# Kernel optimization log

Measured on AMD Instinct MI355X. Metric: run time of the kernel, lower is better.

The kernel has to match this reference:

```python
import jax, jax.numpy as jnp
import numpy as np
from jax import lax

H = 16          # num heads
D_CONV = 4      # causal conv kernel width
NORMALIZER = 16.0
EPS = 1e-5


def _causal_conv_silu(x, w):
    # x: [B, L, D], w: [D, W] depthwise causal conv, then silu
    B, L, D = x.shape
    xp = jnp.pad(x, ((0, 0), (D_CONV - 1, 0), (0, 0)))
    y = sum(xp[:, k:k + L, :] * w[:, k] for k in range(D_CONV))
    return jax.nn.silu(y)


def _gla_scan(q, k, v, gk):
    # q,k,gk: [B,H,L,dk]; v: [B,H,L,dv]
    B, h, L, dk = q.shape
    dv = v.shape[-1]
    qT = jnp.moveaxis(q, 2, 0)
    kT = jnp.moveaxis(k, 2, 0)
    vT = jnp.moveaxis(v, 2, 0)
    gT = jnp.moveaxis(gk, 2, 0)

    def step(S, inp):
        qt, kt, vt, gt = inp  # [B,H,dk] / [B,H,dv]
        S = S * jnp.exp(gt)[..., None] + kt[..., None] * vt[..., None, :]
        ot = jnp.einsum('bhk,bhkv->bhv', qt, S)
        return S, ot

    S0 = jnp.zeros((B, h, dk, dv), q.dtype)
    S, o = lax.scan(step, S0, (qT, kT, vT, gT))
    return jnp.moveaxis(o, 0, 2), S  # [B,H,L,dv], final state


def setup_inputs() -> dict:
    key = jax.random.key(0)
    ks = jax.random.split(key, 9)
    L, B, D = 8192, 8, 1024
    s = lambda fan: 1.0 / np.sqrt(fan)
    return {
        'x': jax.random.normal(ks[0], (L, B, D), jnp.float32),
        'conv_w': jax.random.normal(ks[1], (D, D_CONV), jnp.float32) * s(D_CONV),
        'Wq': jax.random.normal(ks[2], (D, D // 2), jnp.float32) * s(D),
        'Wkg': jax.random.normal(ks[3], (D, D // 2), jnp.float32) * s(D),
        'Wv': jax.random.normal(ks[4], (D, D), jnp.float32) * s(D),
        'Wg': jax.random.normal(ks[5], (D, D), jnp.float32) * s(D),
        'bg': jax.random.normal(ks[6], (D,), jnp.float32) * 0.02,
        'Wout': jax.random.normal(ks[7], (D, D), jnp.float32) * s(D),
        'aug_balance': jnp.zeros((D // 2,), jnp.float32),
    }


def reference(x, conv_w, Wq, Wkg, Wv, Wg, bg, Wout, aug_balance):
    # x: [L, B, D] -> [B, L, D]
    xb = jnp.swapaxes(x, 0, 1)
    xb = _causal_conv_silu(xb, conv_w)

    q = xb @ Wq                      # [B,L,D/2]
    k_gate = xb @ Wkg                # [B,L,D/2]
    v = xb @ Wv                      # [B,L,D]
    g = xb @ Wg + bg                 # [B,L,D]

    gk = jax.nn.log_sigmoid(k_gate) / NORMALIZER
    k = 1.0 - jnp.exp(gk)

    B, L, _ = q.shape
    split = lambda t: t.reshape(B, L, H, -1).transpose(0, 2, 1, 3)  # b h l d
    qh, kh, gkh, vh = split(q), split(k), split(gk), split(v)
    dk = qh.shape[-1]

    # fused_chunk_gla default scale = dk ** -0.5 (applied to q internally)
    o, new_state = _gla_scan(qh * (dk ** -0.5), kh, vh, gkh)

    # meta self-augmentation (uses unscaled q)
    aug = aug_balance.reshape(H, dk)
    aug_w = jnp.einsum('bhlk,hk,bhlk->bhl', qh, aug, kh)
    o = o + jax.nn.sigmoid(aug_w[..., None] * vh)

    # group norm: LayerNorm over head_dim, no affine
    mu = o.mean(-1, keepdims=True)
    var = o.var(-1, keepdims=True)
    o = (o - mu) * lax.rsqrt(var + EPS)

    o = o.transpose(0, 2, 1, 3).reshape(B, L, -1)  # [B,L,D]
    out = (jax.nn.silu(g) * o) @ Wout
    return jnp.swapaxes(out, 0, 1), new_state  # [L,B,D], [B,H,dk,dv]
```

## Files before the change

### kernel.cpp

```cpp
#include <hip/hip_runtime.h>
#include <stdint.h>

typedef __attribute__((ext_vector_type(4))) float f32x4;
typedef _Float16 f16x8 __attribute__((ext_vector_type(8)));
typedef __attribute__((ext_vector_type(8))) unsigned short u16x8;
typedef __attribute__((ext_vector_type(2))) unsigned int u32x2;
typedef unsigned short u16;
typedef unsigned int u32;

#define LSEQ 8192
#define BB 8
#define DD 1024
#define MM 65536
#define NCH 128

__device__ __forceinline__ u16 f2h(float f) {
    _Float16 h = (_Float16)f;
    return *(u16*)&h;
}
__device__ __forceinline__ float h2f(u16 u) {
    _Float16 h = *(_Float16*)&u;
    return (float)h;
}

__device__ __forceinline__ void gload_lds16(const void* g, void* l) {
    __builtin_amdgcn_global_load_lds(
        (const __attribute__((address_space(1))) u32*)g,
        (__attribute__((address_space(3))) u32*)l, 16, 0, 0);
}

__global__ __launch_bounds__(256) void k_conv_silu(const float* __restrict__ x,
                                                   const float* __restrict__ w,
                                                   u16* __restrict__ xb) {
    int m = blockIdx.x;
    int b = m >> 13, l = m & 8191;
    int d0 = threadIdx.x * 4;
    f32x4 wv[4];
#pragma unroll
    for (int j = 0; j < 4; j++) wv[j] = *(const f32x4*)&w[(d0 + j) * 4];
    float acc[4] = {0.f, 0.f, 0.f, 0.f};
#pragma unroll
    for (int kk = 0; kk < 4; kk++) {
        int lp = l - 3 + kk;
        if (lp >= 0) {
            f32x4 xv = *(const f32x4*)&x[((size_t)(lp * BB + b)) * DD + d0];
#pragma unroll
            for (int j = 0; j < 4; j++) acc[j] += xv[j] * wv[j][kk];
        }
    }
    u16 o[4];
#pragma unroll
    for (int j = 0; j < 4; j++) {
        float a = acc[j];
        o[j] = f2h(a / (1.f + __expf(-a)));
    }
    u32x2 pk;
    pk.x = (u32)o[0] | ((u32)o[1] << 16);
    pk.y = (u32)o[2] | ((u32)o[3] << 16);
    *(u32x2*)&xb[(size_t)m * DD + d0] = pk;
}

__global__ __launch_bounds__(256) void k_packW(const float* __restrict__ Wq,
                                               const float* __restrict__ Wkg,
                                               const float* __restrict__ Wv,
                                               const float* __restrict__ Wg,
                                               const float* __restrict__ Wout,
                                               u16* __restrict__ Wcat,
                                               u16* __restrict__ WoutT) {
    int idx = blockIdx.x * 256 + threadIdx.x;
    const int T1 = 3072 * 1024;
    if (idx < T1) {
        int n = idx >> 10, kk = idx & 1023;
        float v;
        if (n < 512)        v = Wq [kk * 512 + n];
        else if (n < 1024)  v = Wkg[kk * 512 + (n - 512)];
        else if (n < 2048)  v = Wv [kk * 1024 + (n - 1024)];
        else                v = Wg [kk * 1024 + (n - 2048)];
        Wcat[idx] = f2h(v);
    } else {
        int j = idx - T1;
        if (j < 1024 * 1024) {
            int n = j >> 10, kk = j & 1023;
            WoutT[j] = f2h(Wout[kk * 1024 + n]);
        }
    }
}

template <int MODE>
__device__ __forceinline__ void epi_frag(f32x4 v, int grow0, int gcol,
                                         u16* __restrict__ qo, u16* __restrict__ gko,
                                         u16* __restrict__ ko, u16* __restrict__ vo,
                                         u16* __restrict__ sgo, const float* __restrict__ bg,
                                         float* __restrict__ out) {
#pragma unroll
    for (int rr = 0; rr < 4; rr++) {
        int grow = grow0 + rr;
        float val = v[rr];
        if (MODE == 1) {
            if (gcol < 512) {
                qo[(size_t)grow * 512 + gcol] = f2h(val);
            } else if (gcol < 1024) {
                float ls = fminf(val, 0.f) - log1pf(__expf(-fabsf(val)));
                float gkv = ls * 0.0625f;
                gko[(size_t)grow * 512 + (gcol - 512)] = f2h(gkv);
                ko [(size_t)grow * 512 + (gcol - 512)] = f2h(-expm1f(gkv));
            } else if (gcol < 2048) {
                vo[(size_t)grow * 1024 + (gcol - 1024)] = f2h(val);
            } else {
                float gg = val + bg[gcol - 2048];
                sgo[(size_t)grow * 1024 + (gcol - 2048)] = f2h(gg / (1.f + __expf(-gg)));
            }
        } else {
            int l = grow & 8191, b = grow >> 13;
            out[((size_t)(l * BB + b)) * DD + gcol] = val;
        }
    }
}

template <int MODE>
__global__ __launch_bounds__(256, 3) void k_gemm_bt(
    const u16* __restrict__ A, const u16* __restrict__ Bt, int nt_tiles,
    u16* __restrict__ qo, u16* __restrict__ gko, u16* __restrict__ ko,
    u16* __restrict__ vo, u16* __restrict__ sgo, const float* __restrict__ bg,
    float* __restrict__ out) {
    const int K = 1024;
    __shared__ __align__(16) u16 Sm[20480];
    int tid = threadIdx.x;
    int w = tid >> 6, lane = tid & 63;
    int wm = w >> 1, wn = w & 1;
    int lr = lane & 15, lk = lane >> 4;

    int xcd = blockIdx.x & 7;
    int cidx = blockIdx.x >> 3;
    int grpsz = nt_tiles * 4;
    int grp = cidx / grpsz;
    int r = cidx - grp * grpsz;
    int ntile = r >> 2;
    int mts_per_chunk = (gridDim.x >> 3) / nt_tiles;
    int mtile = xcd * mts_per_chunk + grp * 4 + (r & 3);
    int m0 = mtile << 8, n0 = ntile << 6;

#define DECL_ACC(MT) f32x4 a##MT##_0 = {0.f,0.f,0.f,0.f}, a##MT##_1 = {0.f,0.f,0.f,0.f};
    DECL_ACC(0) DECL_ACC(1) DECL_ACC(2) DECL_ACC(3)
    DECL_ACC(4) DECL_ACC(5) DECL_ACC(6) DECL_ACC(7)
#undef DECL_ACC

    int row = tid >> 2;
    int sslot = (tid & 3) ^ ((tid >> 3) & 3);
    const u16* gA = A + (size_t)(m0 + row) * K + sslot * 8;
    const u16* gB = Bt + (size_t)(n0 + row) * K + sslot * 8;
    char* lA = (char*)Sm + w * 1024;
    char* lB = (char*)Sm + 16384 + w * 1024;

#define STAGE(TT, OB) { \
    int k1 = (TT) << 5; \
    gload_lds16(gA + k1, lA + (OB)); \
    gload_lds16(gA + (size_t)64 * K + k1, lA + (OB) + 4096); \
    gload_lds16(gA + (size_t)128 * K + k1, lA + (OB) + 8192); \
    gload_lds16(gA + (size_t)192 * K + k1, lA + (OB) + 12288); \
    gload_lds16(gB + k1, lB + (OB)); }

#define MFMA_ROW(MT) { \
    f16x8 av = *(const f16x8*)&As[(wm * 128 + MT * 16 + lr) * 32 + acsl]; \
    a##MT##_0 = __builtin_amdgcn_mfma_f32_16x16x32_f16(av, b0, a##MT##_0, 0, 0, 0); \
    a##MT##_1 = __builtin_amdgcn_mfma_f32_16x16x32_f16(av, b1, a##MT##_1, 0, 0, 0); }

#define COMPUTE() { \
    int acsl = (lk ^ ((lr >> 1) & 3)) * 8; \
    f16x8 b0 = *(const f16x8*)&Bs[(wn * 32 +  0 + lr) * 32 + acsl]; \
    f16x8 b1 = *(const f16x8*)&Bs[(wn * 32 + 16 + lr) * 32 + acsl]; \
    __builtin_amdgcn_s_setprio(1); \
    MFMA_ROW(0) MFMA_ROW(1) MFMA_ROW(2) MFMA_ROW(3) \
    MFMA_ROW(4) MFMA_ROW(5) MFMA_ROW(6) MFMA_ROW(7) \
    __builtin_amdgcn_s_setprio(0); }

    STAGE(0, 0)
    STAGE(1, 20480)

    for (int t = 0; t < 31; ++t) {
        asm volatile("s_waitcnt vmcnt(5)" ::: "memory");
        __builtin_amdgcn_sched_barrier(0);
        __builtin_amdgcn_s_barrier();
        {
            const u16* As = Sm + (t & 1) * 10240;
            const u16* Bs = As + 8192;
            COMPUTE()
        }
        __builtin_amdgcn_s_barrier();
        __builtin_amdgcn_sched_barrier(0);
        if (t < 30) {
            STAGE(t + 2, (t & 1) * 20480)
        }
    }
    asm volatile("s_waitcnt vmcnt(0)" ::: "memory");
    __builtin_amdgcn_sched_barrier(0);
    __builtin_amdgcn_s_barrier();
    {
        const u16* As = Sm + 10240;
        const u16* Bs = As + 8192;
        COMPUTE()
    }
#undef COMPUTE
#undef MFMA_ROW
#undef STAGE

#define EPI_ROW(MT) { \
    int gr0 = m0 + wm * 128 + MT * 16 + lk * 4; \
    epi_frag<MODE>(a##MT##_0, gr0, n0 + wn * 32 +  0 + lr, qo, gko, ko, vo, sgo, bg, out); \
    epi_frag<MODE>(a##MT##_1, gr0, n0 + wn * 32 + 16 + lr, qo, gko, ko, vo, sgo, bg, out); }
    EPI_ROW(0) EPI_ROW(1) EPI_ROW(2) EPI_ROW(3)
    EPI_ROW(4) EPI_ROW(5) EPI_ROW(6) EPI_ROW(7)
#undef EPI_ROW
}

__global__ __launch_bounds__(64) void k_pass1(const u16* __restrict__ gkb,
                                              const u16* __restrict__ kb,
                                              const u16* __restrict__ vb,
                                              float* __restrict__ Mo,
                                              float* __restrict__ eGC) {
    __shared__ __align__(16) float kkT[64 * 32];
    int bhc = blockIdx.x;
    int c = bhc & 127, bh = bhc >> 7;
    int h = bh & 15, b = bh >> 4;
    int m0 = b * LSEQ + c * 64;
    int lane = threadIdx.x;
    if (lane < 32) {
        int i = lane;
        size_t base = (size_t)m0 * 512 + h * 32 + i;
        float G = 0.f;
        for (int t = 0; t < 64; t++) {
            G += h2f(gkb[base + (size_t)t * 512]);
            G = fmaxf(G, -60.f);
            kkT[t * 32 + i] = h2f(kb[base + (size_t)t * 512]) * __expf(-G);
        }
        eGC[bhc * 32 + i] = __expf(G);
    }
    __syncthreads();
    float Ma[32];
#pragma unroll
    for (int i = 0; i < 32; i++) Ma[i] = 0.f;
    size_t vbase = (size_t)m0 * 1024 + h * 64 + lane;
    for (int t = 0; t < 64; t++) {
        float vj = h2f(vb[vbase + (size_t)t * 1024]);
#pragma unroll
        for (int i4 = 0; i4 < 32; i4 += 4) {
            f32x4 kk4 = *(const f32x4*)&kkT[t * 32 + i4];
            Ma[i4 + 0] += kk4[0] * vj;
            Ma[i4 + 1] += kk4[1] * vj;
            Ma[i4 + 2] += kk4[2] * vj;
            Ma[i4 + 3] += kk4[3] * vj;
        }
    }
    size_t mb = (size_t)bhc * 2048 + lane;
#pragma unroll
    for (int i = 0; i < 32; i++) Mo[mb + i * 64] = Ma[i];
}

__global__ __launch_bounds__(64) void k_pass2(float* Mbuf, float* Sbuf,
                                              const float* __restrict__ eGC,
                                              float* __restrict__ state_out, int aliased) {
    int blk = blockIdx.x;
    int bh = blk >> 2, iq = blk & 3;
    int i0 = iq * 8;
    int j = threadIdx.x;
    float S[8];
#pragma unroll
    for (int i = 0; i < 8; i++) S[i] = 0.f;
    for (int c = 0; c < NCH; c++) {
        size_t base = ((size_t)bh * NCH + c) * 2048;
        float mv[8], ev[8];
#pragma unroll
        for (int i = 0; i < 8; i++) mv[i] = Mbuf[base + (i0 + i) * 64 + j];
#pragma unroll
        for (int i = 0; i < 8; i++) ev[i] = eGC[(bh * NCH + c) * 32 + i0 + i];
        if (aliased) { asm volatile("s_waitcnt vmcnt(0)" ::: "memory"); }
#pragma unroll
        for (int i = 0; i < 8; i++) Sbuf[base + (i0 + i) * 64 + j] = S[i];
#pragma unroll
        for (int i = 0; i < 8; i++) S[i] = (S[i] + mv[i]) * ev[i];
    }
    size_t so = (size_t)bh * 2048 + j;
#pragma unroll
    for (int i = 0; i < 8; i++) state_out[so + (i0 + i) * 64] = S[i];
}

__global__ __launch_bounds__(64) void k_pass3(const u16* __restrict__ qb,
                                              const u16* __restrict__ gkb,
                                              const u16* __restrict__ kb,
                                              const u16* __restrict__ vb,
                                              const u16* __restrict__ sgb,
                                              const float* __restrict__ Sbuf,
                                              const float* __restrict__ aug,
                                              u16* __restrict__ PRE) {
    __shared__ __align__(16) u16 qqT[64 * 32];
    __shared__ __align__(16) u16 kkT[64 * 32];
    __shared__ float awl[64];
    int bhc = blockIdx.x;
    int c = bhc & 127, bh = bhc >> 7;
    int h = bh & 15, b = bh >> 4;
    int m0 = b * LSEQ + c * 64;
    int lane = threadIdx.x;
    const float scale = 0.17677669529663689f;
    if (lane < 32) {
        int i = lane;
        size_t base = (size_t)m0 * 512 + h * 32 + i;
        float G = 0.f;
        u16 gk_n = gkb[base], q_n = qb[base], k_n = kb[base];
        for (int t = 0; t < 64; t++) {
            float gkv = h2f(gk_n);
            float qv  = h2f(q_n);
            float kv  = h2f(k_n);
            if (t < 63) {
                size_t nx = base + (size_t)(t + 1) * 512;
                gk_n = gkb[nx]; q_n = qb[nx]; k_n = kb[nx];
            }
            G += gkv;
            G = fmaxf(G, -60.f);
            qqT[t * 32 + i] = f2h(qv * __expf(G) * scale);
            kkT[t * 32 + i] = f2h(kv * __expf(-G));
        }
    }
    {
        int i = lane & 31;
        int th = (lane >> 5) << 5;
        float augi = aug[h * 32 + i];
        size_t base2 = (size_t)m0 * 512 + h * 32 + i;
        u16 q_n = qb[base2 + (size_t)th * 512], k_n = kb[base2 + (size_t)th * 512];
        for (int tt = 0; tt < 32; tt++) {
            int t = tt + th;
            float qv = h2f(q_n);
            float kv = h2f(k_n);
            if (tt < 31) {
                size_t nx = base2 + (size_t)(t + 1) * 512;
                q_n = qb[nx]; k_n = kb[nx];
            }
            float p = qv * kv * augi;
            p += __shfl_xor(p, 1);
            p += __shfl_xor(p, 2);
            p += __shfl_xor(p, 4);
            p += __shfl_xor(p, 8);
            p += __shfl_xor(p, 16);
            if (i == 0) awl[t] = p;
        }
    }
    __syncthreads();
    float T[32];
    size_t sb = (size_t)bhc * 2048 + lane;
#pragma unroll
    for (int i = 0; i < 32; i++) T[i] = Sbuf[sb + i * 64];
    size_t vbase = (size_t)m0 * 1024 + h * 64 + lane;
    u16 v_n = vb[vbase], sg_n = sgb[vbase];
    for (int t = 0; t < 64; t++) {
        float vj  = h2f(v_n);
        float sgj = h2f(sg_n);
        if (t < 63) {
            size_t nx = vbase + (size_t)(t + 1) * 1024;
            v_n = vb[nx]; sg_n = sgb[nx];
        }
        float aw = awl[t];
        float o0 = 0.f, o1 = 0.f, o2 = 0.f, o3 = 0.f;
        u16x8 kk8a = *(const u16x8*)&kkT[t * 32 + 0];
        u16x8 qq8a = *(const u16x8*)&qqT[t * 32 + 0];
        u16x8 kk8b = *(const u16x8*)&kkT[t * 32 + 8];
        u16x8 qq8b = *(const u16x8*)&qqT[t * 32 + 8];
        u16x8 kk8c = *(const u16x8*)&kkT[t * 32 + 16];
        u16x8 qq8c = *(const u16x8*)&qqT[t * 32 + 16];
        u16x8 kk8d = *(const u16x8*)&kkT[t * 32 + 24];
        u16x8 qq8d = *(const u16x8*)&qqT[t * 32 + 24];
#pragma unroll
        for (int e = 0; e < 8; e++) {
            T[e]      += h2f(kk8a[e]) * vj;  o0 += h2f(qq8a[e]) * T[e];
            T[8 + e]  += h2f(kk8b[e]) * vj;  o1 += h2f(qq8b[e]) * T[8 + e];
            T[16 + e] += h2f(kk8c[e]) * vj;  o2 += h2f(qq8c[e]) * T[16 + e];
            T[24 + e] += h2f(kk8d[e]) * vj;  o3 += h2f(qq8d[e]) * T[24 + e];
        }
        float o = (o0 + o1) + (o2 + o3);
        o += 1.f / (1.f + __expf(-aw * vj));
        float s1 = o, s2 = o * o;
#pragma unroll
        for (int msk = 1; msk < 64; msk <<= 1) {
            s1 += __shfl_xor(s1, msk);
            s2 += __shfl_xor(s2, msk);
        }
        float mu = s1 * 0.015625f;
        float var = s2 * 0.015625f - mu * mu;
        float on = (o - mu) * rsqrtf(fmaxf(var, 0.f) + 1e-5f);
        PRE[vbase + (size_t)t * 1024] = f2h(on * sgj);
    }
}

extern "C" void kernel_launch(void* const* d_in, const int* in_sizes, int n_in,
                              void* d_out, int out_size, void* d_ws, size_t ws_size,
                              hipStream_t stream) {
    (void)in_sizes; (void)n_in; (void)out_size;
    const float* x      = (const float*)d_in[0];
    const float* conv_w = (const float*)d_in[1];
    const float* Wq     = (const float*)d_in[2];
    const float* Wkg    = (const float*)d_in[3];
    const float* Wv     = (const float*)d_in[4];
    const float* Wg     = (const float*)d_in[5];
    const float* bg     = (const float*)d_in[6];
    const float* Wout   = (const float*)d_in[7];
    const float* aug    = (const float*)d_in[8];

    char* ws = (char*)d_ws;
    u16*   xb    = (u16*)  (ws + 0);
    u16*   Wcat  = (u16*)  (ws + 134217728);
    u16*   WoutT = (u16*)  (ws + 140509184);
    u16*   qb    = (u16*)  (ws + 142606336);
    u16*   gkb   = (u16*)  (ws + 209715200);
    u16*   kbuf  = (u16*)  (ws + 276824064);
    u16*   sgb   = (u16*)  (ws + 343932928);
    float* Mbuf  = (float*)(ws + 478150656);
    float* eGC   = (float*)(ws + 612368384);
    float* Sb    = (float*)(ws + 614465536);
    const size_t REQ_FULL = 748683264ull;
    int aliased = (ws_size < REQ_FULL) ? 1 : 0;
    float* Sbuf = aliased ? Mbuf : Sb;

    float* out = (float*)d_out;
    float* state_out = out + 67108864;
    u16* vb = (u16*)d_out;

    k_conv_silu<<<dim3(65536), dim3(256), 0, stream>>>(x, conv_w, xb);
    k_packW<<<dim3(16384), dim3(256), 0, stream>>>(Wq, Wkg, Wv, Wg, Wout, Wcat, WoutT);
    k_gemm_bt<1><<<dim3(12288), dim3(256), 0, stream>>>(xb, Wcat, 48,
                                                        qb, gkb, kbuf, vb, sgb, bg, nullptr);
    k_pass1<<<dim3(16384), dim3(64), 0, stream>>>(gkb, kbuf, vb, Mbuf, eGC);
    k_pass2<<<dim3(512), dim3(64), 0, stream>>>(Mbuf, Sbuf, eGC, state_out, aliased);
    k_pass3<<<dim3(16384), dim3(64), 0, stream>>>(qb, gkb, kbuf, vb, sgb, Sbuf, aug, xb );
    k_gemm_bt<2><<<dim3(4096), dim3(256), 0, stream>>>(xb, WoutT, 16,
                                                       nullptr, nullptr, nullptr, nullptr, nullptr, nullptr, out);
}
```

Baseline: 1.691 ms.

## Move gate-scaled q/k and aug-weight prep into pass1, stream precomputed tiles into pass3

Pass1 now computes the cumulative-gate-scaled q and k chunks plus the per-token augmentation weights once, writing them to global scratch. Pass3 loads these with direct global-to-LDS copies instead of re-reading q, gk and k and redoing the exponential scan and shuffle reductions. Sbuf is always aliased onto Mbuf, with an unconditional wait in pass2. This trades extra global writes and reads of the precomputed tiles against removing duplicated serial work in pass3. It also depends on the output buffer being free to hold awl scratch before the final GEMM writes it.

Result: no change. 1.723 ms (+1.9%).

```diff
diff --git a/kernel.cpp b/kernel.cpp
--- a/kernel.cpp
+++ b/kernel.cpp
@@ -213,88 +213,17 @@
 #undef EPI_ROW
 }
 
-__global__ __launch_bounds__(64) void k_pass1(const u16* __restrict__ gkb,
+__global__ __launch_bounds__(64) void k_pass1(const u16* __restrict__ qb,
+                                              const u16* __restrict__ gkb,
                                               const u16* __restrict__ kb,
                                               const u16* __restrict__ vb,
                                               float* __restrict__ Mo,
-                                              float* __restrict__ eGC) {
+                                              float* __restrict__ eGC,
+                                              u16* __restrict__ qqg,
+                                              u16* __restrict__ kkg,
+                                              float* __restrict__ awlg,
+                                              const float* __restrict__ aug) {
     __shared__ __align__(16) float kkT[64 * 32];
-    int bhc = blockIdx.x;
-    int c = bhc & 127, bh = bhc >> 7;
-    int h = bh & 15, b = bh >> 4;
-    int m0 = b * LSEQ + c * 64;
-    int lane = threadIdx.x;
-    if (lane < 32) {
-        int i = lane;
-        size_t base = (size_t)m0 * 512 + h * 32 + i;
-        float G = 0.f;
-        for (int t = 0; t < 64; t++) {
-            G += h2f(gkb[base + (size_t)t * 512]);
-            G = fmaxf(G, -60.f);
-            kkT[t * 32 + i] = h2f(kb[base + (size_t)t * 512]) * __expf(-G);
-        }
-        eGC[bhc * 32 + i] = __expf(G);
-    }
-    __syncthreads();
-    float Ma[32];
-#pragma unroll
-    for (int i = 0; i < 32; i++) Ma[i] = 0.f;
-    size_t vbase = (size_t)m0 * 1024 + h * 64 + lane;
-    for (int t = 0; t < 64; t++) {
-        float vj = h2f(vb[vbase + (size_t)t * 1024]);
-#pragma unroll
-        for (int i4 = 0; i4 < 32; i4 += 4) {
-            f32x4 kk4 = *(const f32x4*)&kkT[t * 32 + i4];
-            Ma[i4 + 0] += kk4[0] * vj;
-            Ma[i4 + 1] += kk4[1] * vj;
-            Ma[i4 + 2] += kk4[2] * vj;
-            Ma[i4 + 3] += kk4[3] * vj;
-        }
-    }
-    size_t mb = (size_t)bhc * 2048 + lane;
-#pragma unroll
-    for (int i = 0; i < 32; i++) Mo[mb + i * 64] = Ma[i];
-}
-
-__global__ __launch_bounds__(64) void k_pass2(float* Mbuf, float* Sbuf,
-                                              const float* __restrict__ eGC,
-                                              float* __restrict__ state_out, int aliased) {
-    int blk = blockIdx.x;
-    int bh = blk >> 2, iq = blk & 3;
-    int i0 = iq * 8;
-    int j = threadIdx.x;
-    float S[8];
-#pragma unroll
-    for (int i = 0; i < 8; i++) S[i] = 0.f;
-    for (int c = 0; c < NCH; c++) {
-        size_t base = ((size_t)bh * NCH + c) * 2048;
-        float mv[8], ev[8];
-#pragma unroll
-        for (int i = 0; i < 8; i++) mv[i] = Mbuf[base + (i0 + i) * 64 + j];
-#pragma unroll
-        for (int i = 0; i < 8; i++) ev[i] = eGC[(bh * NCH + c) * 32 + i0 + i];
-        if (aliased) { asm volatile("s_waitcnt vmcnt(0)" ::: "memory"); }
-#pragma unroll
-        for (int i = 0; i < 8; i++) Sbuf[base + (i0 + i) * 64 + j] = S[i];
-#pragma unroll
-        for (int i = 0; i < 8; i++) S[i] = (S[i] + mv[i]) * ev[i];
-    }
-    size_t so = (size_t)bh * 2048 + j;
-#pragma unroll
-    for (int i = 0; i < 8; i++) state_out[so + (i0 + i) * 64] = S[i];
-}
-
-__global__ __launch_bounds__(64) void k_pass3(const u16* __restrict__ qb,
-                                              const u16* __restrict__ gkb,
-                                              const u16* __restrict__ kb,
-                                              const u16* __restrict__ vb,
-                                              const u16* __restrict__ sgb,
-                                              const float* __restrict__ Sbuf,
-                                              const float* __restrict__ aug,
-                                              u16* __restrict__ PRE) {
-    __shared__ __align__(16) u16 qqT[64 * 32];
-    __shared__ __align__(16) u16 kkT[64 * 32];
-    __shared__ float awl[64];
     int bhc = blockIdx.x;
     int c = bhc & 127, bh = bhc >> 7;
     int h = bh & 15, b = bh >> 4;
@@ -304,6 +233,7 @@
     if (lane < 32) {
         int i = lane;
         size_t base = (size_t)m0 * 512 + h * 32 + i;
+        size_t gq = (size_t)bhc * 2048 + i;
         float G = 0.f;
         u16 gk_n = gkb[base], q_n = qb[base], k_n = kb[base];
         for (int t = 0; t < 64; t++) {
@@ -316,9 +246,12 @@
             }
             G += gkv;
             G = fmaxf(G, -60.f);
-            qqT[t * 32 + i] = f2h(qv * __expf(G) * scale);
-            kkT[t * 32 + i] = f2h(kv * __expf(-G));
-        }
+            float kkf = kv * __expf(-G);
+            kkT[t * 32 + i] = kkf;
+            kkg[gq + t * 32] = f2h(kkf);
+            qqg[gq + t * 32] = f2h(qv * __expf(G) * scale);
+        }
+        eGC[bhc * 32 + i] = __expf(G);
     }
     {
         int i = lane & 31;
@@ -340,16 +273,92 @@
             p += __shfl_xor(p, 4);
             p += __shfl_xor(p, 8);
             p += __shfl_xor(p, 16);
-            if (i == 0) awl[t] = p;
+            if (i == 0) awlg[bhc * 64 + t] = p;
         }
     }
     __syncthreads();
+    float Ma[32];
+#pragma unroll
+    for (int i = 0; i < 32; i++) Ma[i] = 0.f;
+    size_t vbase = (size_t)m0 * 1024 + h * 64 + lane;
+    u16 v_n = vb[vbase];
+    for (int t = 0; t < 64; t++) {
+        float vj = h2f(v_n);
+        if (t < 63) v_n = vb[vbase + (size_t)(t + 1) * 1024];
+#pragma unroll
+        for (int i4 = 0; i4 < 32; i4 += 4) {
+            f32x4 kk4 = *(const f32x4*)&kkT[t * 32 + i4];
+            Ma[i4 + 0] += kk4[0] * vj;
+            Ma[i4 + 1] += kk4[1] * vj;
+            Ma[i4 + 2] += kk4[2] * vj;
+            Ma[i4 + 3] += kk4[3] * vj;
+        }
+    }
+    size_t mb = (size_t)bhc * 2048 + lane;
+#pragma unroll
+    for (int i = 0; i < 32; i++) Mo[mb + i * 64] = Ma[i];
+}
+
+__global__ __launch_bounds__(64) void k_pass2(float* Mbuf, float* Sbuf,
+                                              const float* __restrict__ eGC,
+                                              float* __restrict__ state_out) {
+    int blk = blockIdx.x;
+    int bh = blk >> 2, iq = blk & 3;
+    int i0 = iq * 8;
+    int j = threadIdx.x;
+    float S[8];
+#pragma unroll
+    for (int i = 0; i < 8; i++) S[i] = 0.f;
+    for (int c = 0; c < NCH; c++) {
+        size_t base = ((size_t)bh * NCH + c) * 2048;
+        float mv[8], ev[8];
+#pragma unroll
+        for (int i = 0; i < 8; i++) mv[i] = Mbuf[base + (i0 + i) * 64 + j];
+#pragma unroll
+        for (int i = 0; i < 8; i++) ev[i] = eGC[(bh * NCH + c) * 32 + i0 + i];
+        asm volatile("s_waitcnt vmcnt(0)" ::: "memory");
+#pragma unroll
+        for (int i = 0; i < 8; i++) Sbuf[base + (i0 + i) * 64 + j] = S[i];
+#pragma unroll
+        for (int i = 0; i < 8; i++) S[i] = (S[i] + mv[i]) * ev[i];
+    }
+    size_t so = (size_t)bh * 2048 + j;
+#pragma unroll
+    for (int i = 0; i < 8; i++) state_out[so + (i0 + i) * 64] = S[i];
+}
+
+__global__ __launch_bounds__(64) void k_pass3(const u16* __restrict__ qqg,
+                                              const u16* __restrict__ kkg,
+                                              const float* __restrict__ awlg,
+                                              const u16* __restrict__ vb,
+                                              const u16* __restrict__ sgb,
+                                              const float* __restrict__ Sbuf,
+                                              u16* __restrict__ PRE) {
+    __shared__ __align__(16) u16 qqT[64 * 32];
+    __shared__ __align__(16) u16 kkT[64 * 32];
+    __shared__ float awl[64];
+    int bhc = blockIdx.x;
+    int c = bhc & 127, bh = bhc >> 7;
+    int h = bh & 15, b = bh >> 4;
+    int m0 = b * LSEQ + c * 64;
+    int lane = threadIdx.x;
+    {
+        const u16* gq = qqg + (size_t)bhc * 2048 + lane * 8;
+        const u16* gk = kkg + (size_t)bhc * 2048 + lane * 8;
+#pragma unroll
+        for (int p = 0; p < 4; p++) {
+            gload_lds16(gq + p * 512, (char*)qqT + p * 1024);
+            gload_lds16(gk + p * 512, (char*)kkT + p * 1024);
+        }
+        awl[lane] = awlg[bhc * 64 + lane];
+    }
     float T[32];
     size_t sb = (size_t)bhc * 2048 + lane;
 #pragma unroll
     for (int i = 0; i < 32; i++) T[i] = Sbuf[sb + i * 64];
     size_t vbase = (size_t)m0 * 1024 + h * 64 + lane;
     u16 v_n = vb[vbase], sg_n = sgb[vbase];
+    __syncthreads();
     for (int t = 0; t < 64; t++) {
         float vj  = h2f(v_n);
         float sgj = h2f(sg_n);
@@ -392,7 +401,7 @@
 extern "C" void kernel_launch(void* const* d_in, const int* in_sizes, int n_in,
                               void* d_out, int out_size, void* d_ws, size_t ws_size,
                               hipStream_t stream) {
-    (void)in_sizes; (void)n_in; (void)out_size;
+    (void)in_sizes; (void)n_in; (void)out_size; (void)ws_size;
     const float* x      = (const float*)d_in[0];
     const float* conv_w = (const float*)d_in[1];
     const float* Wq     = (const float*)d_in[2];
@@ -413,22 +422,23 @@
     u16*   sgb   = (u16*)  (ws + 343932928);
     float* Mbuf  = (float*)(ws + 478150656);
     float* eGC   = (float*)(ws + 612368384);
-    float* Sb    = (float*)(ws + 614465536);
-    const size_t REQ_FULL = 748683264ull;
-    int aliased = (ws_size < REQ_FULL) ? 1 : 0;
-    float* Sbuf = aliased ? Mbuf : Sb;
+    u16*   qqg   = (u16*)  (ws + 614465536);
+    u16*   kkg   = (u16*)  (ws + 681574400);
+    float* Sbuf = Mbuf;
 
     float* out = (float*)d_out;
     float* state_out = out + 67108864;
     u16* vb = (u16*)d_out;
+    float* awlg = (float*)((char*)d_out + 134217728);
 
     k_conv_silu<<<dim3(65536), dim3(256), 0, stream>>>(x, conv_w, xb);
     k_packW<<<dim3(16384), dim3(256), 0, stream>>>(Wq, Wkg, Wv, Wg, Wout, Wcat, WoutT);
     k_gemm_bt<1><<<dim3(12288), dim3(256), 0, stream>>>(xb, Wcat, 48,
                                                         qb, gkb, kbuf, vb, sgb, bg, nullptr);
-    k_pass1<<<dim3(16384), dim3(64), 0, stream>>>(gkb, kbuf, vb, Mbuf, eGC);
-    k_pass2<<<dim3(512), dim3(64), 0, stream>>>(Mbuf, Sbuf, eGC, state_out, aliased);
-    k_pass3<<<dim3(16384), dim3(64), 0, stream>>>(qb, gkb, kbuf, vb, sgb, Sbuf, aug, xb );
+    k_pass1<<<dim3(16384), dim3(64), 0, stream>>>(qb, gkb, kbuf, vb, Mbuf, eGC,
+                                                  qqg, kkg, awlg, aug);
+    k_pass2<<<dim3(512), dim3(64), 0, stream>>>(Mbuf, Sbuf, eGC, state_out);
+    k_pass3<<<dim3(16384), dim3(64), 0, stream>>>(qqg, kkg, awlg, vb, sgb, Sbuf, xb );
     k_gemm_bt<2><<<dim3(4096), dim3(256), 0, stream>>>(xb, WoutT, 16,
                                                        nullptr, nullptr, nullptr, nullptr, nullptr, nullptr, out);
 }
```
